# Kernel tuning notes

Hardware: AMD Instinct MI355X
Metric: run time of the kernel (lower is better)

## Reference

```python
import jax, jax.numpy as jnp
import numpy as np

B, S, D = 2, 2048, 2048
H, HD = 16, 128
ROPE_THETA = 10000.0


def _rope_cos_sin(seq_len, head_dim, dtype=jnp.float32):
    inv_freq = 1.0 / (ROPE_THETA ** (jnp.arange(0, head_dim, 2, dtype=jnp.float32) / head_dim))
    t = jnp.arange(seq_len, dtype=jnp.float32)
    freqs = jnp.outer(t, inv_freq)                     # [S, HD/2]
    emb = jnp.concatenate([freqs, freqs], axis=-1)     # [S, HD]
    return jnp.cos(emb).astype(dtype), jnp.sin(emb).astype(dtype)


def _rotate_half(x):
    x1, x2 = jnp.split(x, 2, axis=-1)
    return jnp.concatenate([-x2, x1], axis=-1)


def _apply_rope(x, cos, sin):
    # x: [B, S, H, HD]; cos/sin: [S, HD] -> broadcast over batch and heads
    c = cos[None, :, None, :]
    s = sin[None, :, None, :]
    return x * c + _rotate_half(x) * s


def setup_inputs() -> dict:
    key = jax.random.key(0)
    ks = jax.random.split(key, 6)
    scale = 1.0 / np.sqrt(D)
    hidden_states = jax.random.normal(ks[0], (B, S, D), dtype=jnp.float32)
    # causal additive mask: 0 on/below diagonal, large negative above
    neg = jnp.finfo(jnp.float32).min
    causal = jnp.where(jnp.tril(jnp.ones((S, S), dtype=bool)), 0.0, neg)
    attention_mask = jnp.broadcast_to(causal[None, None, :, :], (B, 1, S, S)).astype(jnp.float32)
    Wq = jax.random.normal(ks[1], (D, D), dtype=jnp.float32) * scale
    Wk = jax.random.normal(ks[2], (D, D), dtype=jnp.float32) * scale
    Wv = jax.random.normal(ks[3], (D, D), dtype=jnp.float32) * scale
    Wo = jax.random.normal(ks[4], (D, D), dtype=jnp.float32) * scale
    return {"hidden_states": hidden_states, "attention_mask": attention_mask,
            "Wq": Wq, "Wk": Wk, "Wv": Wv, "Wo": Wo}


def reference(hidden_states, attention_mask, Wq, Wk, Wv, Wo):
    b, s, d = hidden_states.shape
    # projections (torch Linear: x @ W^T)
    q = (hidden_states @ Wq.T).reshape(b, s, H, HD)
    k = (hidden_states @ Wk.T).reshape(b, s, H, HD)
    v = (hidden_states @ Wv.T).reshape(b, s, H, HD)
    cos, sin = _rope_cos_sin(s, HD, hidden_states.dtype)
    q = _apply_rope(q, cos, sin)
    k = _apply_rope(k, cos, sin)
    # naive attention, [B, H, S, S] scores materialized as in the original
    scores = jnp.einsum('bqhd,bkhd->bhqk', q, k) / np.sqrt(HD)
    scores = scores + attention_mask
    attn = jax.nn.softmax(scores, axis=-1)
    out = jnp.einsum('bhqk,bkhd->bqhd', attn, v).reshape(b, s, d)
    return out @ Wo.T
```

## Files before the change

### kernel.cpp

```cpp
#include <hip/hip_runtime.h>
#include <hip/hip_bf16.h>

typedef __hip_bfloat16 bf16;
typedef __attribute__((ext_vector_type(8))) short s16x8;
typedef __attribute__((ext_vector_type(4))) float f32x4;
typedef __attribute__((ext_vector_type(16))) float f32x16;

#define MFMA16(a, b, c) __builtin_amdgcn_mfma_f32_16x16x32_bf16(a, b, c, 0, 0, 0)
#define MFMA32(a, b, c) __builtin_amdgcn_mfma_f32_32x32x16_bf16(a, b, c, 0, 0, 0)

#define GLL16(gsrc, ldst)                                                                 \
  __builtin_amdgcn_global_load_lds(                                                       \
      (const __attribute__((address_space(1))) unsigned int*)(gsrc),                      \
      (__attribute__((address_space(3))) unsigned int*)(ldst), 16, 0, 0)

#define VMCNT(n) asm volatile("s_waitcnt vmcnt(" #n ")" ::: "memory")
#define BARRIER() __builtin_amdgcn_s_barrier()

static constexpr int S_LEN = 2048;
static constexpr int D_DIM = 2048;
static constexpr int NY = 6144;

union BF4 { ushort4 u; bf16 b[4]; };

__device__ inline unsigned pack2(float a, float b) {
  union { bf16 h[2]; unsigned u; } x;
  x.h[0] = __float2bfloat16(a);
  x.h[1] = __float2bfloat16(b);
  return x.u;
}

__global__ void convert_all(const float* __restrict__ X, const float* __restrict__ Wq,
                            const float* __restrict__ Wk, const float* __restrict__ Wv,
                            const float* __restrict__ Wo, bf16* __restrict__ Xb,
                            bf16* __restrict__ Wb, bf16* __restrict__ Wob,
                            float* __restrict__ cosT, float* __restrict__ sinT) {
  int gid = blockIdx.x * 256 + threadIdx.x;
  if (gid < 6291456) {
    int i4 = gid * 4;
    const float* src;
    bf16* dst;
    int off;
    if (i4 < 8388608) {
      src = X; dst = Xb; off = i4;
    } else {
      int j = i4 - 8388608;
      int seg = j >> 22;
      off = j & 4194303;
      if (seg == 0) { src = Wq; dst = Wb; }
      else if (seg == 1) { src = Wk; dst = Wb + 4194304; }
      else if (seg == 2) { src = Wv; dst = Wb + 8388608; }
      else { src = Wo; dst = Wob; }
    }
    float4 v = *(const float4*)(src + off);
    BF4 o;
    o.b[0] = __float2bfloat16(v.x);
    o.b[1] = __float2bfloat16(v.y);
    o.b[2] = __float2bfloat16(v.z);
    o.b[3] = __float2bfloat16(v.w);
    *(ushort4*)(dst + off) = o.u;
  } else {
    int t4 = (gid - 6291456) * 4;
    if (t4 < 131072) {
#pragma unroll
      for (int k = 0; k < 4; ++k) {
        int i = t4 + k;
        int d = i & 63, s = i >> 6;
        float inv = powf(10000.0f, -(float)d * (1.0f / 64.0f));
        float ang = (float)s * inv;
        cosT[i] = cosf(ang);
        sinT[i] = sinf(ang);
      }
    }
  }
}

__global__ __launch_bounds__(256) void rope_tv(bf16* __restrict__ Y,
                                               const float* __restrict__ cosT,
                                               const float* __restrict__ sinT,
                                               bf16* __restrict__ Vt) {
  __shared__ bf16 tile[32][36];
  const int bid = blockIdx.x;
  const int t = threadIdx.x;
  if (bid < 8192) {
    int idx = bid * 256 + t;
    int quad = idx & 15;
    int h = (idx >> 4) & 15;
    int m = (idx >> 8) & 4095;
    int g = idx >> 20;
    int s = m & (S_LEN - 1);
    int d0 = quad * 4;
    float sc = g ? 1.0f : 0.08838834764831845f * 1.4426950408889634f;
    bf16* p = Y + (size_t)m * NY + g * D_DIM + h * 128 + d0;
    BF4 lo, hi, olo, ohi;
    lo.u = *(const ushort4*)p;
    hi.u = *(const ushort4*)(p + 64);
    float4 c = *(const float4*)(cosT + s * 64 + d0);
    float4 sn = *(const float4*)(sinT + s * 64 + d0);
    float cc[4] = {c.x, c.y, c.z, c.w};
    float ss[4] = {sn.x, sn.y, sn.z, sn.w};
#pragma unroll
    for (int i = 0; i < 4; ++i) {
      float x1 = __bfloat162float(lo.b[i]);
      float x2 = __bfloat162float(hi.b[i]);
      olo.b[i] = __float2bfloat16((x1 * cc[i] - x2 * ss[i]) * sc);
      ohi.b[i] = __float2bfloat16((x2 * cc[i] + x1 * ss[i]) * sc);
    }
    *(ushort4*)p = olo.u;
    *(ushort4*)(p + 64) = ohi.u;
  } else {
    int id = bid - 8192;
    int bx = id & 63, by = (id >> 6) & 3, bh = id >> 8;
    int b = bh >> 4, h = bh & 15;
    int s0 = bx * 32, d0 = by * 32;
    int r = t >> 3;
    int c4 = (t & 7) * 4;
    BF4 in;
    in.u = *(const ushort4*)(Y + (size_t)(b * S_LEN + s0 + r) * NY + 4096 + h * 128 + d0 + c4);
    *(ushort4*)(&tile[r][c4]) = in.u;
    __syncthreads();
    BF4 o;
#pragma unroll
    for (int i = 0; i < 4; ++i) o.b[i] = tile[c4 + i][r];
    *(ushort4*)(Vt + (size_t)bh * 128 * S_LEN + (size_t)(d0 + r) * S_LEN + s0 + c4) = o.u;
  }
}

__device__ inline void storeC(float* p, float v) { *p = v; }
__device__ inline void storeC(bf16* p, float v) { *p = __float2bfloat16(v); }

__global__ __launch_bounds__(512, 2) void gemm256(const bf16* __restrict__ A,
                                                  const bf16* __restrict__ Bm,
                                                  bf16* __restrict__ C, int K, int lda,
                                                  int ldb, int ldc, int mt) {
  __shared__ __align__(16) char lds[131072];
  char* A0buf = lds;
  char* B0buf = lds + 32768;
  char* A1buf = lds + 65536;
  char* B1buf = lds + 98304;
  const int tid = threadIdx.x;
  const int lane = tid & 63;
  const int w = tid >> 6;
  const int wm = w >> 2, wn = w & 3;
  const int l15 = lane & 15, lh4 = lane >> 4;
  const int xr = l15 & 7;
  const int xo0 = ((lh4 ^ xr) << 4);
  const int xo1 = (((4 + lh4) ^ xr) << 4);

  const int nwg = gridDim.x;
  const int bid = blockIdx.x;
  const int swz = (bid & 7) * (nwg >> 3) + (bid >> 3);
  const int bm = swz % mt, bn = swz / mt;
  const int row0 = bm * 256, col0 = bn * 256;

  const int srow8 = lane >> 3;
  const int scol = ((lane & 7) ^ srow8) * 8;
  const bf16* gA_s = A + (size_t)(row0 + w * 8 + srow8) * lda + scol;
  const bf16* gB_s = Bm + (size_t)(col0 + (w >> 2) * 64 + (w & 3) * 8 + srow8) * ldb + scol;
  const int ldst = w * 1024;

#define STAGE_A(bufa, rh, k0)                                                     \
  {                                                                               \
    GLL16(gA_s + (size_t)((rh)*64) * lda + (k0), (bufa) + (rh)*16384 + ldst);     \
    GLL16(gA_s + (size_t)((rh)*64 + 128) * lda + (k0),                            \
          (bufa) + (rh)*16384 + 8192 + ldst);                                     \
  }
#define STAGE_B(bufb, ch, k0)                                                     \
  {                                                                               \
    GLL16(gB_s + (size_t)((ch)*32) * ldb + (k0), (bufb) + (ch)*16384 + ldst);     \
    GLL16(gB_s + (size_t)((ch)*32 + 128) * ldb + (k0),                            \
          (bufb) + (ch)*16384 + 8192 + ldst);                                     \
  }

  f32x4 acc[8][4];
#pragma unroll
  for (int i = 0; i < 8; ++i)
#pragma unroll
    for (int j = 0; j < 4; ++j) acc[i][j] = (f32x4){0.f, 0.f, 0.f, 0.f};

  s16x8 af[4][2];
  s16x8 bfr[2][2];

#define READ_AH(bufa, rh)                                                         \
  _Pragma("unroll") for (int ii = 0; ii < 4; ++ii) {                              \
    const char* p_ = (bufa) + (rh)*16384 + (wm * 64 + ii * 16 + l15) * 128;       \
    af[ii][0] = *(const s16x8*)(p_ + xo0);                                        \
    af[ii][1] = *(const s16x8*)(p_ + xo1);                                        \
  }
#define READ_BH(bufb, ch)                                                         \
  _Pragma("unroll") for (int jj = 0; jj < 2; ++jj) {                              \
    const char* p_ = (bufb) + (ch)*16384 + (wn * 32 + jj * 16 + l15) * 128;       \
    bfr[jj][0] = *(const s16x8*)(p_ + xo0);                                       \
    bfr[jj][1] = *(const s16x8*)(p_ + xo1);                                       \
  }
#define QUAD(rh, ch)                                                              \
  __builtin_amdgcn_s_setprio(1);                                                  \
  _Pragma("unroll") for (int jj = 0; jj < 2; ++jj)                                \
  _Pragma("unroll") for (int ii = 0; ii < 4; ++ii)                                \
  _Pragma("unroll") for (int ks = 0; ks < 2; ++ks)                                \
      acc[(rh)*4 + ii][(ch)*2 + jj] =                                             \
          MFMA16(af[ii][ks], bfr[jj][ks], acc[(rh)*4 + ii][(ch)*2 + jj]);         \
  __builtin_amdgcn_s_setprio(0);

  STAGE_A(A0buf, 0, 0);
  STAGE_B(B0buf, 0, 0);
  STAGE_B(B0buf, 1, 0);
  STAGE_A(A0buf, 1, 0);
  STAGE_A(A1buf, 0, 64);
  STAGE_B(B1buf, 1, 64);
  STAGE_A(A1buf, 1, 64);
  VMCNT(6);
  BARRIER();

  const int NI = K >> 7;
  for (int i = 0; i < NI; ++i) {
    const int kT1 = (2 * i + 1) << 6;
    const int kT2 = (2 * i + 2) << 6;
    const int kT3 = (2 * i + 3) << 6;
    const bool nl = (i + 1 < NI);
    READ_AH(A0buf, 0);
    READ_BH(B0buf, 0);
    STAGE_B(B1buf, 0, kT1);
    BARRIER();
    QUAD(0, 0);
    BARRIER();
    READ_BH(B0buf, 1);
    if (nl) STAGE_A(A0buf, 0, kT2);
    BARRIER();
    QUAD(0, 1);
    BARRIER();
    READ_AH(A0buf, 1);
    if (nl) STAGE_B(B0buf, 1, kT2);
    BARRIER();
    QUAD(1, 1);
    BARRIER();
    READ_BH(B0buf, 0);
    if (nl) STAGE_A(A0buf, 1, kT2);
    BARRIER();
    QUAD(1, 0);
    if (nl) { VMCNT(6); } else { VMCNT(0); }
    BARRIER();
    READ_AH(A1buf, 0);
    READ_BH(B1buf, 0);
    if (nl) STAGE_B(B0buf, 0, kT2);
    BARRIER();
    QUAD(0, 0);
    BARRIER();
    READ_BH(B1buf, 1);
    if (nl) STAGE_A(A1buf, 0, kT3);
    BARRIER();
    QUAD(0, 1);
    BARRIER();
    READ_AH(A1buf, 1);
    if (nl) STAGE_B(B1buf, 1, kT3);
    BARRIER();
    QUAD(1, 1);
    BARRIER();
    READ_BH(B1buf, 0);
    if (nl) STAGE_A(A1buf, 1, kT3);
    BARRIER();
    QUAD(1, 0);
    if (nl) { VMCNT(6); }
    BARRIER();
  }
#undef STAGE_A
#undef STAGE_B
#undef READ_AH
#undef READ_BH
#undef QUAD

#pragma unroll
  for (int ri = 0; ri < 8; ++ri)
#pragma unroll
    for (int cj = 0; cj < 4; ++cj) {
      int gr = row0 + wm * 128 + ri * 16 + lh4 * 4;
      int gc = col0 + wn * 64 + cj * 16 + l15;
#pragma unroll
      for (int rr = 0; rr < 4; ++rr)
        C[(size_t)(gr + rr) * ldc + gc] = __float2bfloat16(acc[ri][cj][rr]);
    }
}

template <typename OutT>
__global__ __launch_bounds__(512, 2) void gemm_fine(const bf16* __restrict__ A,
                                                    const bf16* __restrict__ Bm,
                                                    OutT* __restrict__ C, int K, int lda,
                                                    int ldb, int ldc, int mt) {
  __shared__ __align__(16) char lds[147456];
  char* b0 = lds;
  char* b1 = lds + 49152;
  char* b2 = lds + 98304;
  const int tid = threadIdx.x;
  const int lane = tid & 63;
  const int w = tid >> 6;
  const int wm = w >> 2, wn = w & 3;
  const int l15 = lane & 15, lh4 = lane >> 4;
  const int xr = l15 & 7;
  const int xo0 = ((lh4 ^ xr) << 4);
  const int xo1 = (((4 + lh4) ^ xr) << 4);

  const int nwg = gridDim.x;
  const int bid = blockIdx.x;
  const int swz = (bid & 7) * (nwg >> 3) + (bid >> 3);
  const int bm = swz % mt, bn = swz / mt;
  const int row0 = bm * 128, col0 = bn * 256;

  const int srow = w * 8 + (lane >> 3);
  const int scol = ((lane & 7) ^ (lane >> 3)) * 8;
  const bf16* gA = A + (size_t)(row0 + srow) * lda + scol;
  const bf16* gB = Bm + (size_t)(col0 + srow) * ldb + scol;
  const int ldst = w * 1024;

  f32x4 acc[4][4];
#pragma unroll
  for (int i = 0; i < 4; ++i)
#pragma unroll
    for (int j = 0; j < 4; ++j) acc[i][j] = (f32x4){0.f, 0.f, 0.f, 0.f};

  s16x8 af[4], bfr[4];

#define PH_READ(BUF, XO)                                                          \
  _Pragma("unroll") for (int ii = 0; ii < 4; ++ii)                                \
      af[ii] = *(const s16x8*)((BUF) + (wm * 64 + ii * 16 + l15) * 128 + (XO));   \
  _Pragma("unroll") for (int jj = 0; jj < 4; ++jj)                                \
      bfr[jj] = *(const s16x8*)((BUF) + 16384 + (wn * 64 + jj * 16 + l15) * 128 + (XO));
#define PH_FMA()                                                                  \
  __builtin_amdgcn_s_setprio(1);                                                  \
  _Pragma("unroll") for (int jj = 0; jj < 4; ++jj)                                \
  _Pragma("unroll") for (int ii = 0; ii < 4; ++ii)                                \
      acc[ii][jj] = MFMA16(af[ii], bfr[jj], acc[ii][jj]);                         \
  __builtin_amdgcn_s_setprio(0);
#define STAGE_T(BUF, kS)                                                          \
  GLL16(gA + (kS), (BUF) + ldst);                                                 \
  GLL16(gA + (size_t)64 * lda + (kS), (BUF) + 8192 + ldst);                       \
  GLL16(gB + (kS), (BUF) + 16384 + ldst);                                         \
  GLL16(gB + (size_t)64 * ldb + (kS), (BUF) + 24576 + ldst);                      \
  GLL16(gB + (size_t)128 * ldb + (kS), (BUF) + 32768 + ldst);                     \
  GLL16(gB + (size_t)192 * ldb + (kS), (BUF) + 40960 + ldst);
#define TILE_MAIN(RBUF, SBUF, kS)                                                 \
  PH_READ(RBUF, xo0);                                                             \
  GLL16(gA + (kS), (SBUF) + ldst);                                                \
  GLL16(gA + (size_t)64 * lda + (kS), (SBUF) + 8192 + ldst);                      \
  GLL16(gB + (kS), (SBUF) + 16384 + ldst);                                        \
  BARRIER();                                                                      \
  PH_FMA();                                                                       \
  BARRIER();                                                                      \
  PH_READ(RBUF, xo1);                                                             \
  GLL16(gB + (size_t)64 * ldb + (kS), (SBUF) + 24576 + ldst);                     \
  GLL16(gB + (size_t)128 * ldb + (kS), (SBUF) + 32768 + ldst);                    \
  GLL16(gB + (size_t)192 * ldb + (kS), (SBUF) + 40960 + ldst);                    \
  BARRIER();                                                                      \
  PH_FMA();                                                                       \
  VMCNT(6);                                                                       \
  BARRIER();

  STAGE_T(b0, 0);
  STAGE_T(b1, 64);
  VMCNT(6);
  BARRIER();

  const int NT = K >> 6;
  for (int t = 0; t < NT - 2; t += 3) {
    TILE_MAIN(b0, b2, (size_t)(t + 2) * 64);
    TILE_MAIN(b1, b0, (size_t)(t + 3) * 64);
    TILE_MAIN(b2, b1, (size_t)(t + 4) * 64);
  }
  PH_READ(b0, xo0);
  BARRIER();
  PH_FMA();
  BARRIER();
  PH_READ(b0, xo1);
  BARRIER();
  PH_FMA();
  VMCNT(0);
  BARRIER();
  PH_READ(b1, xo0);
  BARRIER();
  PH_FMA();
  BARRIER();
  PH_READ(b1, xo1);
  BARRIER();
  PH_FMA();
#undef PH_READ
#undef PH_FMA
#undef STAGE_T
#undef TILE_MAIN

#pragma unroll
  for (int mi = 0; mi < 4; ++mi)
#pragma unroll
    for (int ni = 0; ni < 4; ++ni) {
      int gr = row0 + wm * 64 + mi * 16 + lh4 * 4;
      int gc = col0 + wn * 64 + ni * 16 + l15;
#pragma unroll
      for (int rr = 0; rr < 4; ++rr)
        storeC(&C[(size_t)(gr + rr) * ldc + gc], acc[mi][ni][rr]);
    }
}

__global__ __launch_bounds__(256, 2) void attn_fwd(const bf16* __restrict__ Y,
                                                   const bf16* __restrict__ Vt,
                                                   bf16* __restrict__ At) {
  __shared__ __align__(16) char smem[65536];

  const int idx = blockIdx.x;
  const int qt = 15 - (idx >> 5);
  const int bh = idx & 31;
  const int b = bh >> 4, h = bh & 15;
  const int tid = threadIdx.x;
  const int lane = tid & 63;
  const int w = tid >> 6;
  const int l31 = lane & 31;
  const int hi = lane >> 5;
  const int q0w = qt * 128 + w * 32;
  const int q = q0w + l31;

  s16x8 qf[8];
  {
    const bf16* qb = Y + (size_t)(b * S_LEN + q) * NY + h * 128 + hi * 8;
#pragma unroll
    for (int s = 0; s < 8; ++s) qf[s] = *(const s16x8*)(qb + s * 16);
  }

  f32x16 O[4];
#pragma unroll
  for (int d = 0; d < 4; ++d)
#pragma unroll
    for (int e = 0; e < 16; ++e) O[d][e] = 0.f;
  float m_run = -3.0e38f, l_run = 0.f;

  const bf16* Kbase = Y + (size_t)(b * S_LEN) * NY + 2048 + h * 128;
  const bf16* Vbase = Vt + (size_t)bh * 128 * S_LEN;
  const int tmax = 2 * qt + 1;

  const int rk_ = w * 4 + (lane >> 4);
  const int ck_ = lane & 15;
  const int dv_ = w * 8 + (lane >> 3);
  const int cv_ = lane & 7;

#define STAGE_KV(T, BASE)                                                         \
  {                                                                               \
    const int kv0s = (T)*64;                                                      \
    _Pragma("unroll") for (int j = 0; j < 4; ++j) {                               \
      int rk = j * 16 + rk_;                                                      \
      GLL16(Kbase + (size_t)(kv0s + rk) * NY + ((ck_ ^ (rk & 15)) * 8),           \
            (BASE) + (j * 4096 + w * 1024));                                      \
      int dv = j * 32 + dv_;                                                      \
      GLL16(Vbase + (size_t)dv * S_LEN + kv0s + ((cv_ ^ (dv & 7)) * 8),           \
            (BASE) + 16384 + (j * 4096 + w * 1024));                              \
    }                                                                             \
  }

  STAGE_KV(0, smem);

  for (int t = 0; t <= tmax; ++t) {
    const int kv0 = t * 64;
    const char* cur = smem + (t & 1) * 32768;
    BARRIER();
    if (t < tmax) {
      STAGE_KV(t + 1, smem + ((t + 1) & 1) * 32768);
      VMCNT(8);
    } else {
      VMCNT(0);
    }
    BARRIER();
    if (kv0 > q0w + 31) continue;

    float sv[32];
#pragma unroll
    for (int tt = 0; tt < 2; ++tt) {
      f32x16 sa;
#pragma unroll
      for (int e = 0; e < 16; ++e) sa[e] = 0.f;
      const int rk = tt * 32 + l31;
      const char* kr = cur + rk * 256;
      const int xr = (rk & 15) << 4;
#pragma unroll
      for (int s = 0; s < 8; ++s) {
        s16x8 kf = *(const s16x8*)(kr + ((s * 32 + hi * 16) ^ xr));
        sa = MFMA32(kf, qf[s], sa);
      }
#pragma unroll
      for (int e = 0; e < 16; ++e) sv[tt * 16 + e] = sa[e];
    }

    if (kv0 + 63 > q0w) {
#pragma unroll
      for (int tt = 0; tt < 2; ++tt)
#pragma unroll
        for (int r = 0; r < 16; ++r) {
          int kvr = kv0 + tt * 32 + (r & 3) + 8 * (r >> 2) + 4 * hi;
          if (kvr > q) sv[tt * 16 + r] = -3.0e38f;
        }
    }

    float mx[16];
#pragma unroll
    for (int i = 0; i < 16; ++i) mx[i] = fmaxf(sv[i], sv[i + 16]);
#pragma unroll
    for (int st = 8; st >= 1; st >>= 1)
#pragma unroll
      for (int i = 0; i < 8; ++i)
        if (i < st) mx[i] = fmaxf(mx[i], mx[i + st]);
    float pmax = fmaxf(mx[0], __shfl_xor(mx[0], 32, 64));

    bool need = pmax > m_run + 11.54f;
    if (__any(need)) {
      float newm = fmaxf(m_run, pmax);
      float ef = exp2f(m_run - newm);
      m_run = newm;
      l_run *= ef;
#pragma unroll
      for (int d = 0; d < 4; ++d)
#pragma unroll
        for (int e = 0; e < 16; ++e) O[d][e] *= ef;
    }

    float rsum = 0.f;
#pragma unroll
    for (int i = 0; i < 32; ++i) {
      sv[i] = exp2f(sv[i] - m_run);
      rsum += sv[i];
    }
    rsum += __shfl_xor(rsum, 32, 64);
    l_run += rsum;

    unsigned pw[4][4];
#pragma unroll
    for (int tt = 0; tt < 2; ++tt) {
      const int bs = tt * 16;
      unsigned x01 = pack2(sv[bs + 0], sv[bs + 1]);
      unsigned x23 = pack2(sv[bs + 2], sv[bs + 3]);
      unsigned x45 = pack2(sv[bs + 4], sv[bs + 5]);
      unsigned x67 = pack2(sv[bs + 6], sv[bs + 7]);
      unsigned y01 = pack2(sv[bs + 8], sv[bs + 9]);
      unsigned y23 = pack2(sv[bs + 10], sv[bs + 11]);
      unsigned y45 = pack2(sv[bs + 12], sv[bs + 13]);
      unsigned y67 = pack2(sv[bs + 14], sv[bs + 15]);
      asm volatile("v_permlane32_swap_b32 %0, %1" : "+v"(x01), "+v"(x45));
      asm volatile("v_permlane32_swap_b32 %0, %1" : "+v"(x23), "+v"(x67));
      asm volatile("v_permlane32_swap_b32 %0, %1" : "+v"(y01), "+v"(y45));
      asm volatile("v_permlane32_swap_b32 %0, %1" : "+v"(y23), "+v"(y67));
      pw[tt * 2][0] = x01;
      pw[tt * 2][1] = x23;
      pw[tt * 2][2] = x45;
      pw[tt * 2][3] = x67;
      pw[tt * 2 + 1][0] = y01;
      pw[tt * 2 + 1][1] = y23;
      pw[tt * 2 + 1][2] = y45;
      pw[tt * 2 + 1][3] = y67;
    }

#pragma unroll
    for (int dt = 0; dt < 4; ++dt) {
      const int d = dt * 32 + l31;
      const char* vr = cur + 16384 + d * 128;
      const int xv = (d & 7) << 4;
#pragma unroll
      for (int sl = 0; sl < 4; ++sl) {
        s16x8 vf = *(const s16x8*)(vr + ((sl * 32 + hi * 16) ^ xv));
        union { unsigned u[4]; s16x8 v; } pb;
        pb.u[0] = pw[sl][0];
        pb.u[1] = pw[sl][1];
        pb.u[2] = pw[sl][2];
        pb.u[3] = pw[sl][3];
        O[dt] = MFMA32(vf, pb.v, O[dt]);
      }
    }
  }
#undef STAGE_KV

  __syncthreads();
  const float inv = 1.0f / l_run;
  {
    const int orow = w * 32 + l31;
    const int xo = (orow & 15) << 4;
    char* obase = (char*)smem + orow * 256;
#pragma unroll
    for (int dt = 0; dt < 4; ++dt)
#pragma unroll
      for (int r = 0; r < 16; ++r) {
        int d = dt * 32 + (r & 3) + 8 * (r >> 2) + 4 * hi;
        *(bf16*)(obase + ((d * 2) ^ xo)) = __float2bfloat16(O[dt][r] * inv);
      }
  }
  __syncthreads();
  bf16* dst = At + (size_t)(b * S_LEN + qt * 128) * D_DIM + h * 128;
#pragma unroll
  for (int j = 0; j < 8; ++j) {
    int id = j * 256 + tid;
    int rr = id >> 4, cc = id & 15;
    int4 val = *(const int4*)((char*)smem + rr * 256 + ((cc * 16) ^ ((rr & 15) << 4)));
    *(int4*)(dst + (size_t)rr * D_DIM + cc * 8) = val;
  }
}

extern "C" void kernel_launch(void* const* d_in, const int* in_sizes, int n_in,
                              void* d_out, int out_size, void* d_ws, size_t ws_size,
                              hipStream_t stream) {
  const float* X = (const float*)d_in[0];
  const float* Wq = (const float*)d_in[2];
  const float* Wk = (const float*)d_in[3];
  const float* Wv = (const float*)d_in[4];
  const float* Wo = (const float*)d_in[5];
  float* out = (float*)d_out;
  char* ws = (char*)d_ws;

  bf16* Xb = (bf16*)(ws);
  bf16* Wb = (bf16*)(ws + 16777216);
  bf16* Wob = (bf16*)(ws + 41943040);
  bf16* Y = (bf16*)(ws + 50331648);
  bf16* Vt = (bf16*)(ws + 100663296);
  bf16* At = (bf16*)(ws + 117440512);
  float* cosT = (float*)(ws + 134217728);
  float* sinT = (float*)(ws + 134742016);

  convert_all<<<24704, 256, 0, stream>>>(X, Wq, Wk, Wv, Wo, Xb, Wb, Wob, cosT, sinT);

  gemm256<<<256, 512, 0, stream>>>(Xb, Wb, Y, 2048, 2048, 2048, 6144, 16);
  gemm_fine<bf16><<<256, 512, 0, stream>>>(Xb, Wb + (size_t)4096 * 2048, Y + 4096,
                                           2048, 2048, 2048, 6144, 32);
  rope_tv<<<16384, 256, 0, stream>>>(Y, cosT, sinT, Vt);
  attn_fwd<<<512, 256, 0, stream>>>(Y, Vt, At);
  gemm_fine<float><<<256, 512, 0, stream>>>(At, Wob, out, 2048, 2048, 2048, 2048, 32);
}
```

Baseline: 247.8 us.

## Reorder attention q-tile schedule, raise wave priority around MFMAs, tree-reduce softmax

Blocks with index 256 and above now visit query tiles in ascending order while the first 256 keep descending order, changing how causal work is balanced across the grid. The QK^T and PV MFMA loops are wrapped in s_setprio(1)/s_setprio(0) so waves issuing matrix ops are favoured over waves doing softmax. The row max and row sum are computed as balanced trees instead of a serial chain, shortening the dependency chains. Wave priority can starve other waves, and the grid-order change only matters if the launch has more than 256 blocks.

Measured after the change: 245.8 us. Within noise of the previous version (-0.8%).

```diff
diff --git a/kernel.cpp b/kernel.cpp
--- a/kernel.cpp
+++ b/kernel.cpp
@@ -404,7 +404,7 @@
   __shared__ __align__(16) char smem[65536];
 
   const int idx = blockIdx.x;
-  const int qt = 15 - (idx >> 5);
+  const int qt = (idx < 256) ? (15 - (idx >> 5)) : ((idx - 256) >> 5);
   const int bh = idx & 31;
   const int b = bh >> 4, h = bh & 15;
   const int tid = threadIdx.x;
@@ -475,11 +475,13 @@
       const int rk = tt * 32 + l31;
       const char* kr = cur + rk * 256;
       const int xr = (rk & 15) << 4;
+      __builtin_amdgcn_s_setprio(1);
 #pragma unroll
       for (int s = 0; s < 8; ++s) {
         s16x8 kf = *(const s16x8*)(kr + ((s * 32 + hi * 16) ^ xr));
         sa = MFMA32(kf, qf[s], sa);
       }
+      __builtin_amdgcn_s_setprio(0);
 #pragma unroll
       for (int e = 0; e < 16; ++e) sv[tt * 16 + e] = sa[e];
     }
@@ -494,15 +496,13 @@
         }
     }
 
-    float mx[16];
-#pragma unroll
-    for (int i = 0; i < 16; ++i) mx[i] = fmaxf(sv[i], sv[i + 16]);
-#pragma unroll
-    for (int st = 8; st >= 1; st >>= 1)
-#pragma unroll
-      for (int i = 0; i < 8; ++i)
-        if (i < st) mx[i] = fmaxf(mx[i], mx[i + st]);
-    float pmax = fmaxf(mx[0], __shfl_xor(mx[0], 32, 64));
+    float m8[8];
+#pragma unroll
+    for (int i = 0; i < 8; ++i)
+      m8[i] = fmaxf(fmaxf(sv[i], sv[i + 8]), fmaxf(sv[i + 16], sv[i + 24]));
+    float m2a = fmaxf(fmaxf(m8[0], m8[1]), fmaxf(m8[2], m8[3]));
+    float m2b = fmaxf(fmaxf(m8[4], m8[5]), fmaxf(m8[6], m8[7]));
+    float pmax = fmaxf(fmaxf(m2a, m2b), __shfl_xor(fmaxf(m2a, m2b), 32, 64));
 
     bool need = pmax > m_run + 11.54f;
     if (__any(need)) {
@@ -516,12 +516,18 @@
         for (int e = 0; e < 16; ++e) O[d][e] *= ef;
     }
 
-    float rsum = 0.f;
-#pragma unroll
-    for (int i = 0; i < 32; ++i) {
-      sv[i] = exp2f(sv[i] - m_run);
-      rsum += sv[i];
-    }
+#pragma unroll
+    for (int i = 0; i < 32; ++i) sv[i] = exp2f(sv[i] - m_run);
+    float s16v[16];
+#pragma unroll
+    for (int i = 0; i < 16; ++i) s16v[i] = sv[i] + sv[i + 16];
+    float s8v[8];
+#pragma unroll
+    for (int i = 0; i < 8; ++i) s8v[i] = s16v[i] + s16v[i + 8];
+    float s4v[4];
+#pragma unroll
+    for (int i = 0; i < 4; ++i) s4v[i] = s8v[i] + s8v[i + 4];
+    float rsum = (s4v[0] + s4v[1]) + (s4v[2] + s4v[3]);
     rsum += __shfl_xor(rsum, 32, 64);
     l_run += rsum;
 
@@ -556,6 +562,7 @@
       const int d = dt * 32 + l31;
       const char* vr = cur + 16384 + d * 128;
       const int xv = (d & 7) << 4;
+      __builtin_amdgcn_s_setprio(1);
 #pragma unroll
       for (int sl = 0; sl < 4; ++sl) {
         s16x8 vf = *(const s16x8*)(vr + ((sl * 32 + hi * 16) ^ xv));
@@ -566,6 +573,7 @@
         pb.u[3] = pw[sl][3];
         O[dt] = MFMA32(vf, pb.v, O[dt]);
       }
+      __builtin_amdgcn_s_setprio(0);
     }
   }
 #undef STAGE_KV
```
